# Kernel optimization log

Hardware: AMD Instinct MI355X
Metric: run time of the kernel (lower is better)

Reference implementation:

```python
import jax, jax.numpy as jnp
import numpy as np

N = 20000   # nodes
E = 320000  # edges
G = 64      # graphs in batch
IN = 256    # in_dim
H = 256     # hidden_dim1
C = 2       # n_classes


def setup_inputs() -> dict:
    key = jax.random.key(0)
    ks = jax.random.split(key, 12)
    h = jax.random.normal(ks[0], (N, IN), jnp.float32)
    src = jax.random.randint(ks[1], (E,), 0, N)
    dst = jax.random.randint(ks[2], (E,), 0, N)
    graph_id = jnp.sort(jax.random.randint(ks[3], (N,), 0, G))
    s_in = 1.0 / np.sqrt(IN)
    s_h = 1.0 / np.sqrt(H)
    W_conv = jax.random.normal(ks[4], (IN, H), jnp.float32) * s_in
    b_conv = jnp.zeros((H,), jnp.float32)
    w_gate = jax.random.normal(ks[5], (H, 1), jnp.float32) * s_h
    b_gate = jnp.zeros((1,), jnp.float32)
    W1 = jax.random.normal(ks[6], (H, H), jnp.float32) * s_h
    b1 = jnp.zeros((H,), jnp.float32)
    W2 = jax.random.normal(ks[7], (H, C), jnp.float32) * s_h
    b2 = jnp.zeros((C,), jnp.float32)
    return dict(h=h, src=src, dst=dst, graph_id=graph_id, W_conv=W_conv,
                b_conv=b_conv, w_gate=w_gate, b_gate=b_gate, W1=W1, b1=b1,
                W2=W2, b2=b2)


def reference(h, src, dst, graph_id, W_conv, b_conv, w_gate, b_gate, W1, b1, W2, b2):
    ones_e = jnp.ones((E,), jnp.float32)
    # DGL GraphConv, norm='both': D_out^-1/2 on source, D_in^-1/2 on dest
    deg_out = jax.ops.segment_sum(ones_e, src, num_segments=N)
    deg_in = jax.ops.segment_sum(ones_e, dst, num_segments=N)
    hn = h * jax.lax.rsqrt(jnp.maximum(deg_out, 1.0))[:, None]
    hn = hn @ W_conv                       # [N, H] (weight applied before aggregation)
    agg = jax.ops.segment_sum(hn[src], dst, num_segments=N)  # gather + scatter-add
    agg = agg * jax.lax.rsqrt(jnp.maximum(deg_in, 1.0))[:, None] + b_conv
    hr = jax.nn.relu(agg)                  # F.relu after conv1
    # GlobalAttentionPooling: per-graph segment softmax over gate scores
    gate = hr @ w_gate + b_gate            # [N, 1]
    gmax = jax.ops.segment_max(gate, graph_id, num_segments=G)
    e = jnp.exp(gate - gmax[graph_id])
    denom = jax.ops.segment_sum(e, graph_id, num_segments=G)
    att = e / denom[graph_id]              # [N, 1] attention weights (g2)
    hg = jax.ops.segment_sum(att * hr, graph_id, num_segments=G)  # [G, H]
    # classifier heads (dropout is identity at inference)
    a2 = hg @ W1 + b1
    a3 = a2 @ W2 + b2
    return jax.nn.sigmoid(a3), att, hg
```

## Files before the change

kernel.cpp:

```cpp
#include <hip/hip_runtime.h>
#include <hip/hip_bf16.h>
#include <hip/hip_fp16.h>
#include <math.h>

#define NN 20000
#define EE 320000
#define GG 64
#define IND 256
#define HD 256
#define CC 2

#define HRB 32
#define EPB (EE/HRB)
#define NH  (NN/2)

typedef __hip_bfloat16 bf16;
typedef __attribute__((ext_vector_type(8))) short short8;
typedef __attribute__((ext_vector_type(4))) float f32x4;

__device__ __forceinline__ float b2f(bf16 x){ return __bfloat162float(x); }
__device__ __forceinline__ float bits2f(unsigned short b){
    union{ float f; unsigned u; } v; v.u = ((unsigned)b) << 16; return v.f;
}
__device__ __forceinline__ short f2bs(float x){
    union{ bf16 b; short s; } u; u.b = __float2bfloat16(x); return u.s;
}
__device__ __forceinline__ float ldf3(const void* p, size_t i, int c){
    if (c == 1) return b2f(((const bf16*)p)[i]);
    if (c == 2) return __half2float(((const __half*)p)[i]);
    return ((const float*)p)[i];
}
__device__ __forceinline__ int idec(const void* p, int i, int c){
    if (c == 1) return (int)(((const long long*)p)[i]);
    if (c == 2) return (int)(((const float*)p)[i]);
    if (c == 3) return (int)__half2float(((const __half*)p)[i]);
    return ((const int*)p)[i];
}
__device__ __forceinline__ int wdetect_wave(const unsigned short* p, int t){
    unsigned u = p[2*t];
    int e8 = (u >> 7) & 0xFF;
    int e5 = (u >> 10) & 0x1F;
    int nz = __popcll(__ballot(u != 0));
    int cb = __popcll(__ballot(e8 >= 100 && e8 <= 141));
    int cf = __popcll(__ballot(e5 >= 4 && e5 <= 22));
    return (nz < 8) ? 0 : (cb >= 60) ? 1 : ((cf >= 60) ? 2 : 0);
}

#define ZBLK 8
#define DETB (9 + IND)
__global__ __launch_bounds__(256) void k_detect(const void* src, const void* dst,
                         const void* gid,
                         const unsigned short* h, const unsigned short* Wc,
                         const unsigned short* wg, const unsigned short* W1,
                         const unsigned short* W2, const unsigned short* bc,
                         int* icode, int* dcode, int* zero_base,
                         bf16* __restrict__ Wb){
    int blk = blockIdx.x;
    int t = threadIdx.x;
    if (blk < 3){
        if (t >= 64) return;
        const void* buf = (blk == 0) ? src : (blk == 1) ? dst : gid;
        int n     = (blk == 2) ? NN : EE;
        int bound = (blk == 2) ? GG : NN;
        long long v64 = ((const long long*)buf)[n/8 + t];
        unsigned long long bad64 = __ballot(v64 < 0 || v64 >= (long long)bound);
        int v32 = ((const int*)buf)[n/4 + t];
        unsigned long long bad32 = __ballot(v32 < 0 || v32 >= bound);
        float f32v = __uint_as_float(((const unsigned*)buf)[n/4 + t]);
        unsigned long long badf32 = __ballot(!(f32v >= 0.f && f32v < (float)bound));
        float f16v = __half2float(((const __half*)buf)[n/2 + t]);
        unsigned long long badf16 = __ballot(!(f16v >= 0.f && f16v < (float)bound));
        if (t == 0)
            icode[blk] = (bad64 == 0ull) ? 1 : ((bad32 == 0ull) ? 0 :
                         ((badf32 == 0ull) ? 2 : ((badf16 == 0ull) ? 3 : 0)));
    } else if (blk < 9){
        if (t >= 64) return;
        int b = blk - 3;
        const unsigned short* p = b==0?h:b==1?Wc:b==2?wg:b==3?W1:b==4?W2:bc;
        int code = wdetect_wave(p, t);
        if (t == 0) dcode[b] = code;
    } else if (blk < DETB){
        int k = blk - 9;
        __shared__ int scode;
        if (t < 64){
            int code = wdetect_wave(Wc, t);
            if (t == 0) scode = code;
        }
        __syncthreads();
        int c = scode;
        Wb[(size_t)t*IND + k] = __float2bfloat16(ldf3(Wc, (size_t)k*HD + t, c));
    } else {
        int idx = (blk - DETB)*256 + t;
        const int total = GG*HD;
        for (int i = idx; i < total; i += ZBLK*256) zero_base[i] = 0;
    }
}

#define GEMMB (NN/32)
__global__ __launch_bounds__(256) void k_prepgemm(const void* __restrict__ h,
                                                  const bf16* __restrict__ Wb,
                                                  const void* __restrict__ src_r,
                                                  const void* __restrict__ dst_r,
                                                  const int* __restrict__ icode,
                                                  const int* __restrict__ dcode,
                                                  int* __restrict__ pout,
                                                  int* __restrict__ pin,
                                                  bf16* __restrict__ hn){
    __shared__ int shm[NH];
    int blk = blockIdx.x;
    int tid = threadIdx.x;
    if (blk >= GEMMB){
        int hb = blk - GEMMB;
        int hr = hb >> 2, role = (hb >> 1) & 1, half = hb & 1;
        for (int i = tid; i < NH; i += 256) shm[i] = 0;
        __syncthreads();
        const void* arr = role ? dst_r : src_r;
        int code = icode[role];
        int base = hr*EPB;
        for (int e = base + tid; e < base + EPB; e += 256){
            int v = idec(arr, e, code);
            int vh = v - half*NH;
            if ((unsigned)vh < NH) atomicAdd(&shm[vh], 1);
        }
        __syncthreads();
        int* dst_part = (role ? pin : pout) + (size_t)hr*NN + half*NH;
        for (int i = tid; i < NH; i += 256) dst_part[i] = shm[i];
        return;
    }
    unsigned short* tile = (unsigned short*)shm;
    int fh = dcode[0];
    int wave = tid >> 6, lane = tid & 63;
    int q = lane >> 4, mr = lane & 15;
    int row0 = blk * 32;
    int ncol0 = wave * 64;
    f32x4 acc[2][4] = {};
    const float* hf = (const float*)h;
    #pragma unroll
    for (int k0 = 0; k0 < IND; k0 += 32){
        short8 a[2], b[4];
        if (fh == 0){
            #pragma unroll
            for (int mi = 0; mi < 2; mi++){
                int r = row0 + mi*16 + mr;
                const float4* p = (const float4*)(hf + (size_t)r*IND + k0 + q*8);
                float4 v0 = p[0], v1 = p[1];
                a[mi][0] = f2bs(v0.x); a[mi][1] = f2bs(v0.y);
                a[mi][2] = f2bs(v0.z); a[mi][3] = f2bs(v0.w);
                a[mi][4] = f2bs(v1.x); a[mi][5] = f2bs(v1.y);
                a[mi][6] = f2bs(v1.z); a[mi][7] = f2bs(v1.w);
            }
        } else {
            #pragma unroll
            for (int mi = 0; mi < 2; mi++){
                int r = row0 + mi*16 + mr;
                #pragma unroll
                for (int j = 0; j < 8; j++)
                    a[mi][j] = f2bs(ldf3(h, (size_t)r*IND + k0 + q*8 + j, fh));
            }
        }
        #pragma unroll
        for (int ni = 0; ni < 4; ni++)
            b[ni] = *reinterpret_cast<const short8*>(
                        Wb + (size_t)(ncol0 + ni*16 + mr)*IND + k0 + q*8);
        #pragma unroll
        for (int mi = 0; mi < 2; mi++)
            #pragma unroll
            for (int ni = 0; ni < 4; ni++)
                acc[mi][ni] = __builtin_amdgcn_mfma_f32_16x16x32_bf16(
                                  a[mi], b[ni], acc[mi][ni], 0, 0, 0);
    }
    #pragma unroll
    for (int mi = 0; mi < 2; mi++){
        int rowb = mi*16 + q*4;
        #pragma unroll
        for (int r = 0; r < 4; r++){
            int row = rowb + r;
            #pragma unroll
            for (int ni = 0; ni < 4; ni++)
                tile[row*260 + ncol0 + ni*16 + mr] =
                    (unsigned short)f2bs(acc[mi][ni][r]);
        }
    }
    __syncthreads();
    #pragma unroll
    for (int p = 0; p < 4; p++){
        int s = p*256 + tid;
        int row = s >> 5;
        int c8 = (s & 31) * 8;
        short8 v = *reinterpret_cast<const short8*>(&tile[row*260 + c8]);
        *reinterpret_cast<short8*>(hn + (size_t)(row0 + row)*HD + c8) = v;
    }
}

__global__ __launch_bounds__(256) void k_red(const void* __restrict__ gid_r,
                                             const int* __restrict__ icode,
                                             int* __restrict__ pout,
                                             int* __restrict__ pin,
                                             float* __restrict__ rs_o,
                                             float* __restrict__ rs_i,
                                             int* __restrict__ cnt_in,
                                             int* __restrict__ gid_i){
    int n = blockIdx.x*256 + threadIdx.x;
    if (n >= NN) return;
    int so = 0;
    #pragma unroll 8
    for (int hr = 0; hr < HRB; hr++) so += pout[(size_t)hr*NN + n];
    rs_o[n] = rsqrtf(fmaxf((float)so, 1.f));
    int pre = 0;
    #pragma unroll 8
    for (int hr = 0; hr < HRB; hr++){
        int v = pin[(size_t)hr*NN + n];
        pin[(size_t)hr*NN + n] = pre;
        pre += v;
    }
    cnt_in[n] = pre;
    rs_i[n] = rsqrtf(fmaxf((float)pre, 1.f));
    gid_i[n] = idec(gid_r, n, icode[2]);
}

__global__ __launch_bounds__(1024) void k_scan(const int* __restrict__ cnt_in,
                                               const int* __restrict__ gid,
                                               int* __restrict__ row_start,
                                               int* gstart, int* gend){
    int t = threadIdx.x;
    __shared__ int part[1024];
    const int per = (NN + 1023)/1024;
    int lo = t*per, hi = min(lo+per, NN);
    int s = 0;
    for (int i = lo; i < hi; i++) s += cnt_in[i];
    part[t] = s; __syncthreads();
    for (int off = 1; off < 1024; off <<= 1){
        int v = (t >= off) ? part[t-off] : 0;
        __syncthreads();
        part[t] += v;
        __syncthreads();
    }
    int base = part[t] - s;
    for (int i = lo; i < hi; i++){ row_start[i] = base; base += cnt_in[i]; }
    if (t == 1023) row_start[NN] = part[1023];
    __shared__ int ls[GG+1];
    if (t <= GG){
        int a = 0, b = NN;
        while (a < b){
            int mid = (a + b) >> 1;
            if (gid[mid] < t) a = mid + 1; else b = mid;
        }
        ls[t] = a;
    }
    __syncthreads();
    if (t < GG){ gstart[t] = ls[t]; gend[t] = ls[t+1]; }
}

__global__ __launch_bounds__(256) void k_fill(const void* src_r, const void* dst_r,
                       const int* __restrict__ icode,
                       const int* __restrict__ row_start,
                       const int* __restrict__ pin,
                       int* __restrict__ csr_src){
    __shared__ int lr[NH];
    int blk = blockIdx.x, t = threadIdx.x;
    int hr = blk >> 1, half = blk & 1;
    for (int i = t; i < NH; i += 256) lr[i] = 0;
    __syncthreads();
    int c0 = icode[0], c1 = icode[1];
    int base = hr*EPB;
    const int* pre = pin + (size_t)hr*NN;
    for (int e = base + t; e < base + EPB; e += 256){
        int s = idec(src_r, e, c0);
        int d = idec(dst_r, e, c1);
        if ((unsigned)s >= NN || (unsigned)d >= NN) continue;
        int dh = d - half*NH;
        if ((unsigned)dh < NH){
            int r = atomicAdd(&lr[dh], 1);
            csr_src[row_start[d] + pre[d] + r] = s;
        }
    }
}

__global__ __launch_bounds__(256) void k_gather(const bf16* __restrict__ hn,
                                                const float* __restrict__ rs_out,
                                                const float* __restrict__ rs_in,
                                                const int* __restrict__ row_start,
                                                const int* __restrict__ csr_src,
                                                const void* __restrict__ b_conv,
                                                const void* __restrict__ w_gate,
                                                const void* __restrict__ b_gate,
                                                const int* __restrict__ dcode,
                                                float* __restrict__ hr,
                                                float* __restrict__ gate){
    int wave = threadIdx.x >> 6, lane = threadIdx.x & 63;
    int n = blockIdx.x*4 + wave;
    if (n >= NN) return;
    int lo = row_start[n], hi = row_start[n+1];
    int half = lane >> 5, l2 = lane & 31;
    float a0=0.f,a1=0.f,a2=0.f,a3=0.f,a4=0.f,a5=0.f,a6=0.f,a7=0.f;
    int j = lo;
    for (; j + 8 <= hi; j += 8){
        int sA = csr_src[j+0+half], sB = csr_src[j+2+half];
        int sC = csr_src[j+4+half], sD = csr_src[j+6+half];
        float rA = rs_out[sA], rB = rs_out[sB], rC = rs_out[sC], rD = rs_out[sD];
        short8 uA = *reinterpret_cast<const short8*>(hn + (size_t)sA*HD + l2*8);
        short8 uB = *reinterpret_cast<const short8*>(hn + (size_t)sB*HD + l2*8);
        short8 uC = *reinterpret_cast<const short8*>(hn + (size_t)sC*HD + l2*8);
        short8 uD = *reinterpret_cast<const short8*>(hn + (size_t)sD*HD + l2*8);
        a0 = fmaf(rA, bits2f((unsigned short)uA[0]),
             fmaf(rB, bits2f((unsigned short)uB[0]),
             fmaf(rC, bits2f((unsigned short)uC[0]),
             fmaf(rD, bits2f((unsigned short)uD[0]), a0))));
        a1 = fmaf(rA, bits2f((unsigned short)uA[1]),
             fmaf(rB, bits2f((unsigned short)uB[1]),
             fmaf(rC, bits2f((unsigned short)uC[1]),
             fmaf(rD, bits2f((unsigned short)uD[1]), a1))));
        a2 = fmaf(rA, bits2f((unsigned short)uA[2]),
             fmaf(rB, bits2f((unsigned short)uB[2]),
             fmaf(rC, bits2f((unsigned short)uC[2]),
             fmaf(rD, bits2f((unsigned short)uD[2]), a2))));
        a3 = fmaf(rA, bits2f((unsigned short)uA[3]),
             fmaf(rB, bits2f((unsigned short)uB[3]),
             fmaf(rC, bits2f((unsigned short)uC[3]),
             fmaf(rD, bits2f((unsigned short)uD[3]), a3))));
        a4 = fmaf(rA, bits2f((unsigned short)uA[4]),
             fmaf(rB, bits2f((unsigned short)uB[4]),
             fmaf(rC, bits2f((unsigned short)uC[4]),
             fmaf(rD, bits2f((unsigned short)uD[4]), a4))));
        a5 = fmaf(rA, bits2f((unsigned short)uA[5]),
             fmaf(rB, bits2f((unsigned short)uB[5]),
             fmaf(rC, bits2f((unsigned short)uC[5]),
             fmaf(rD, bits2f((unsigned short)uD[5]), a5))));
        a6 = fmaf(rA, bits2f((unsigned short)uA[6]),
             fmaf(rB, bits2f((unsigned short)uB[6]),
             fmaf(rC, bits2f((unsigned short)uC[6]),
             fmaf(rD, bits2f((unsigned short)uD[6]), a6))));
        a7 = fmaf(rA, bits2f((unsigned short)uA[7]),
             fmaf(rB, bits2f((unsigned short)uB[7]),
             fmaf(rC, bits2f((unsigned short)uC[7]),
             fmaf(rD, bits2f((unsigned short)uD[7]), a7))));
    }
    for (; j + 2 <= hi; j += 2){
        int s = csr_src[j+half];
        float r = rs_out[s];
        short8 u = *reinterpret_cast<const short8*>(hn + (size_t)s*HD + l2*8);
        a0 = fmaf(r, bits2f((unsigned short)u[0]), a0);
        a1 = fmaf(r, bits2f((unsigned short)u[1]), a1);
        a2 = fmaf(r, bits2f((unsigned short)u[2]), a2);
        a3 = fmaf(r, bits2f((unsigned short)u[3]), a3);
        a4 = fmaf(r, bits2f((unsigned short)u[4]), a4);
        a5 = fmaf(r, bits2f((unsigned short)u[5]), a5);
        a6 = fmaf(r, bits2f((unsigned short)u[6]), a6);
        a7 = fmaf(r, bits2f((unsigned short)u[7]), a7);
    }
    if (j < hi && half == 0){
        int s = csr_src[j];
        float r = rs_out[s];
        short8 u = *reinterpret_cast<const short8*>(hn + (size_t)s*HD + l2*8);
        a0 = fmaf(r, bits2f((unsigned short)u[0]), a0);
        a1 = fmaf(r, bits2f((unsigned short)u[1]), a1);
        a2 = fmaf(r, bits2f((unsigned short)u[2]), a2);
        a3 = fmaf(r, bits2f((unsigned short)u[3]), a3);
        a4 = fmaf(r, bits2f((unsigned short)u[4]), a4);
        a5 = fmaf(r, bits2f((unsigned short)u[5]), a5);
        a6 = fmaf(r, bits2f((unsigned short)u[6]), a6);
        a7 = fmaf(r, bits2f((unsigned short)u[7]), a7);
    }
    float send0 = half ? a0 : a4;
    float send1 = half ? a1 : a5;
    float send2 = half ? a2 : a6;
    float send3 = half ? a3 : a7;
    float recv0 = __shfl_xor(send0, 32);
    float recv1 = __shfl_xor(send1, 32);
    float recv2 = __shfl_xor(send2, 32);
    float recv3 = __shfl_xor(send3, 32);
    float tot0 = (half ? a4 : a0) + recv0;
    float tot1 = (half ? a5 : a1) + recv1;
    float tot2 = (half ? a6 : a2) + recv2;
    float tot3 = (half ? a7 : a3) + recv3;
    int db = dcode[5], fg = dcode[2];
    float rsn = rs_in[n];
    int c = l2*8 + half*4;
    float v0 = fmaxf(fmaf(tot0, rsn, ldf3(b_conv, c+0, db)), 0.f);
    float v1 = fmaxf(fmaf(tot1, rsn, ldf3(b_conv, c+1, db)), 0.f);
    float v2 = fmaxf(fmaf(tot2, rsn, ldf3(b_conv, c+2, db)), 0.f);
    float v3 = fmaxf(fmaf(tot3, rsn, ldf3(b_conv, c+3, db)), 0.f);
    float4 fv; fv.x = v0; fv.y = v1; fv.z = v2; fv.w = v3;
    *(float4*)(hr + (size_t)n*HD + c) = fv;
    float g = v0*ldf3(w_gate, c+0, fg) + v1*ldf3(w_gate, c+1, fg)
            + v2*ldf3(w_gate, c+2, fg) + v3*ldf3(w_gate, c+3, fg);
    #pragma unroll
    for (int off = 32; off; off >>= 1) g += __shfl_down(g, off);
    if (lane == 0) gate[n] = g + ldf3(b_gate, 0, db);
}

__global__ __launch_bounds__(256) void k_softhg(const float* __restrict__ gate,
                                                const float* __restrict__ hr,
                                                const int* __restrict__ gstart,
                                                const int* __restrict__ gend,
                                                float* __restrict__ hg,
                                                float* __restrict__ out_att){
    int g = blockIdx.x >> 3, part = blockIdx.x & 7;
    int t = threadIdx.x, lane = t & 63, wid = t >> 6;
    int lo = gstart[g], hi = gend[g], len = hi - lo;
    if (len <= 0) return;
    __shared__ float red[4];
    float m = -INFINITY;
    for (int n = lo + t; n < hi; n += 256) m = fmaxf(m, gate[n]);
    #pragma unroll
    for (int off = 32; off; off >>= 1) m = fmaxf(m, __shfl_xor(m, off));
    if (lane == 0) red[wid] = m;
    __syncthreads();
    m = fmaxf(fmaxf(red[0], red[1]), fmaxf(red[2], red[3]));
    __syncthreads();
    float s = 0.f;
    for (int n = lo + t; n < hi; n += 256) s += expf(gate[n] - m);
    #pragma unroll
    for (int off = 32; off; off >>= 1) s += __shfl_xor(s, off);
    if (lane == 0) red[wid] = s;
    __syncthreads();
    s = red[0] + red[1] + red[2] + red[3];
    float inv = 1.f / s;
    int chunk = (len + 7) >> 3;
    int plo = lo + part*chunk, phi = min(plo + chunk, hi);
    if (plo >= phi) return;
    for (int n = plo + t; n < phi; n += 256)
        out_att[n] = expf(gate[n] - m) * inv;
    float a0 = 0.f, a1 = 0.f, a2 = 0.f, a3 = 0.f;
    int r = plo;
    for (; r + 4 <= phi; r += 4){
        float w0 = expf(gate[r+0] - m) * inv;
        float w1 = expf(gate[r+1] - m) * inv;
        float w2 = expf(gate[r+2] - m) * inv;
        float w3 = expf(gate[r+3] - m) * inv;
        a0 = fmaf(w0, hr[(size_t)(r+0)*HD + t], a0);
        a1 = fmaf(w1, hr[(size_t)(r+1)*HD + t], a1);
        a2 = fmaf(w2, hr[(size_t)(r+2)*HD + t], a2);
        a3 = fmaf(w3, hr[(size_t)(r+3)*HD + t], a3);
    }
    for (; r < phi; r++)
        a0 = fmaf(expf(gate[r] - m) * inv, hr[(size_t)r*HD + t], a0);
    atomicAdd(&hg[g*HD + t], (a0 + a1) + (a2 + a3));
}

__global__ __launch_bounds__(256) void k_cls(const float* __restrict__ hg,
                                             const void* __restrict__ W1,
                                             const void* __restrict__ b1,
                                             const void* __restrict__ W2,
                                             const void* __restrict__ b2,
                                             const int* __restrict__ dcode,
                                             float* __restrict__ out0,
                                             float* __restrict__ out_hg){
    int f1 = dcode[3], f2 = dcode[4], db = dcode[5];
    int g = blockIdx.x, tid = threadIdx.x;
    __shared__ float hs[256];
    float hv = hg[g*HD + tid];
    hs[tid] = hv;
    out_hg[g*HD + tid] = hv;
    __syncthreads();
    float acc = ldf3(b1, tid, db);
    if (f1 == 1){
        const bf16* w = (const bf16*)W1;
        for (int k = 0; k < HD; k++) acc += hs[k]*b2f(w[(size_t)k*HD + tid]);
    } else if (f1 == 2){
        const __half* w = (const __half*)W1;
        for (int k = 0; k < HD; k++) acc += hs[k]*__half2float(w[(size_t)k*HD + tid]);
    } else {
        const float* w = (const float*)W1;
        for (int k = 0; k < HD; k++) acc += hs[k]*w[(size_t)k*HD + tid];
    }
    float p0 = acc * ldf3(W2, tid*CC + 0, f2);
    float p1 = acc * ldf3(W2, tid*CC + 1, f2);
    __shared__ float r0[256], r1[256];
    r0[tid] = p0; r1[tid] = p1; __syncthreads();
    for (int s = 128; s; s >>= 1){
        if (tid < s){ r0[tid] += r0[tid+s]; r1[tid] += r1[tid+s]; }
        __syncthreads();
    }
    if (tid == 0){
        out0[g*CC+0] = 1.f/(1.f + expf(-(r0[0] + ldf3(b2, 0, db))));
        out0[g*CC+1] = 1.f/(1.f + expf(-(r1[0] + ldf3(b2, 1, db))));
    }
}

extern "C" void kernel_launch(void* const* d_in, const int* in_sizes, int n_in,
                              void* d_out, int out_size, void* d_ws, size_t ws_size,
                              hipStream_t stream) {
    const void* h      = d_in[0];
    const void* src_r  = d_in[1];
    const void* dst_r  = d_in[2];
    const void* gid_r  = d_in[3];
    const void* W_conv = d_in[4];
    const void* b_conv = d_in[5];
    const void* w_gate = d_in[6];
    const void* b_gate = d_in[7];
    const void* W1     = d_in[8];
    const void* b1     = d_in[9];
    const void* W2     = d_in[10];
    const void* b2     = d_in[11];

    float* out     = (float*)d_out;
    float* out0    = out;
    float* out_att = out + GG*CC;
    float* out_hg  = out + GG*CC + NN;

    char* w = (char*)d_ws;
    float* hr   = (float*)w;  w += (size_t)NN*HD*sizeof(float);
    bf16*  hn   = (bf16*)w;   w += (size_t)NN*HD*sizeof(bf16);
    bf16*  Wb   = (bf16*)w;   w += (size_t)IND*HD*sizeof(bf16);
    float* rs_o = (float*)w;  w += (size_t)NN*sizeof(float);
    float* rs_i = (float*)w;  w += (size_t)NN*sizeof(float);
    float* gate = (float*)w;  w += (size_t)NN*sizeof(float);
    int* gstart = (int*)w;    w += GG*sizeof(int);
    int* gend   = (int*)w;    w += GG*sizeof(int);
    int* dcode  = (int*)w;    w += 8*sizeof(int);
    int* icode  = (int*)w;    w += 8*sizeof(int);
    int* gid_i  = (int*)w;    w += (size_t)NN*sizeof(int);
    int* cnt_in = (int*)w;    w += (size_t)NN*sizeof(int);
    float* hg   = (float*)w;  w += (size_t)GG*HD*sizeof(float);
    int* rowst  = (int*)w;    w += (size_t)(NN+1)*sizeof(int);
    int* csr    = (int*)w;    w += (size_t)EE*sizeof(int);
    int* pout   = (int*)w;    w += (size_t)HRB*NN*sizeof(int);
    int* pin    = (int*)w;    w += (size_t)HRB*NN*sizeof(int);

    k_detect<<<DETB + ZBLK, 256, 0, stream>>>(src_r, dst_r, gid_r,
                                     (const unsigned short*)h, (const unsigned short*)W_conv,
                                     (const unsigned short*)w_gate, (const unsigned short*)W1,
                                     (const unsigned short*)W2, (const unsigned short*)b_conv,
                                     icode, dcode, hg ? (int*)hg : nullptr, Wb);

    k_prepgemm<<<GEMMB + HRB*4, 256, 0, stream>>>(h, Wb, src_r, dst_r,
                                                  icode, dcode, pout, pin, hn);

    k_red<<<(NN+255)/256, 256, 0, stream>>>(gid_r, icode, pout, pin,
                                            rs_o, rs_i, cnt_in, gid_i);

    k_scan<<<1, 1024, 0, stream>>>(cnt_in, gid_i, rowst, gstart, gend);

    k_fill<<<HRB*2, 256, 0, stream>>>(src_r, dst_r, icode, rowst, pin, csr);

    k_gather<<<(NN+3)/4, 256, 0, stream>>>(hn, rs_o, rs_i, rowst, csr,
                                           b_conv, w_gate, b_gate, dcode, hr, gate);

    k_softhg<<<GG*8, 256, 0, stream>>>(gate, hr, gstart, gend, hg, out_att);

    k_cls<<<GG, 256, 0, stream>>>(hg, W1, b1, W2, b2, dcode, out0, out_hg);
}
```

Before: 223.2 us.

## Move degree histograms into detect kernel and fuse degree reduction with GEMM

The per-chunk degree histogram blocks move from the GEMM kernel into the detect kernel, and each block detects the index dtype itself. The degree reduction kernel is merged into the GEMM launch as extra blocks, which removes one kernel launch and its serialization point. The detect kernel now declares 40KB of shared memory for every block, which may lower its occupancy.

```diff
diff --git a/kernel.cpp b/kernel.cpp
--- a/kernel.cpp
+++ b/kernel.cpp
@@ -45,6 +45,18 @@
     int cf = __popcll(__ballot(e5 >= 4 && e5 <= 22));
     return (nz < 8) ? 0 : (cb >= 60) ? 1 : ((cf >= 60) ? 2 : 0);
 }
+__device__ __forceinline__ int idetect_wave(const void* buf, int n, int bound, int t){
+    long long v64 = ((const long long*)buf)[n/8 + t];
+    unsigned long long bad64 = __ballot(v64 < 0 || v64 >= (long long)bound);
+    int v32 = ((const int*)buf)[n/4 + t];
+    unsigned long long bad32 = __ballot(v32 < 0 || v32 >= bound);
+    float f32v = __uint_as_float(((const unsigned*)buf)[n/4 + t]);
+    unsigned long long badf32 = __ballot(!(f32v >= 0.f && f32v < (float)bound));
+    float f16v = __half2float(((const __half*)buf)[n/2 + t]);
+    unsigned long long badf16 = __ballot(!(f16v >= 0.f && f16v < (float)bound));
+    return (bad64 == 0ull) ? 1 : ((bad32 == 0ull) ? 0 :
+           ((badf32 == 0ull) ? 2 : ((badf16 == 0ull) ? 3 : 0)));
+}
 
 #define ZBLK 8
 #define DETB (9 + IND)
@@ -54,7 +66,10 @@
                          const unsigned short* wg, const unsigned short* W1,
                          const unsigned short* W2, const unsigned short* bc,
                          int* icode, int* dcode, int* zero_base,
-                         bf16* __restrict__ Wb){
+                         bf16* __restrict__ Wb,
+                         int* __restrict__ pout, int* __restrict__ pin){
+    __shared__ int shm[NH];
+    __shared__ int scode;
     int blk = blockIdx.x;
     int t = threadIdx.x;
     if (blk < 3){
@@ -62,17 +77,8 @@
         const void* buf = (blk == 0) ? src : (blk == 1) ? dst : gid;
         int n     = (blk == 2) ? NN : EE;
         int bound = (blk == 2) ? GG : NN;
-        long long v64 = ((const long long*)buf)[n/8 + t];
-        unsigned long long bad64 = __ballot(v64 < 0 || v64 >= (long long)bound);
-        int v32 = ((const int*)buf)[n/4 + t];
-        unsigned long long bad32 = __ballot(v32 < 0 || v32 >= bound);
-        float f32v = __uint_as_float(((const unsigned*)buf)[n/4 + t]);
-        unsigned long long badf32 = __ballot(!(f32v >= 0.f && f32v < (float)bound));
-        float f16v = __half2float(((const __half*)buf)[n/2 + t]);
-        unsigned long long badf16 = __ballot(!(f16v >= 0.f && f16v < (float)bound));
-        if (t == 0)
-            icode[blk] = (bad64 == 0ull) ? 1 : ((bad32 == 0ull) ? 0 :
-                         ((badf32 == 0ull) ? 2 : ((badf16 == 0ull) ? 3 : 0)));
+        int code = idetect_wave(buf, n, bound, t);
+        if (t == 0) icode[blk] = code;
     } else if (blk < 9){
         if (t >= 64) return;
         int b = blk - 3;
@@ -81,7 +87,6 @@
         if (t == 0) dcode[b] = code;
     } else if (blk < DETB){
         int k = blk - 9;
-        __shared__ int scode;
         if (t < 64){
             int code = wdetect_wave(Wc, t);
             if (t == 0) scode = code;
@@ -89,45 +94,69 @@
         __syncthreads();
         int c = scode;
         Wb[(size_t)t*IND + k] = __float2bfloat16(ldf3(Wc, (size_t)k*HD + t, c));
+    } else if (blk < DETB + HRB*4){
+        int hb = blk - DETB;
+        int hr = hb >> 2, role = (hb >> 1) & 1, half = hb & 1;
+        const void* arr = role ? dst : src;
+        if (t < 64){
+            int code = idetect_wave(arr, EE, NN, t);
+            if (t == 0) scode = code;
+        }
+        for (int i = t; i < NH; i += 256) shm[i] = 0;
+        __syncthreads();
+        int code = scode;
+        int base = hr*EPB;
+        for (int e = base + t; e < base + EPB; e += 256){
+            int v = idec(arr, e, code);
+            int vh = v - half*NH;
+            if ((unsigned)vh < NH) atomicAdd(&shm[vh], 1);
+        }
+        __syncthreads();
+        int* dst_part = (role ? pin : pout) + (size_t)hr*NN + half*NH;
+        for (int i = t; i < NH; i += 256) dst_part[i] = shm[i];
     } else {
-        int idx = (blk - DETB)*256 + t;
+        int idx = (blk - (DETB + HRB*4))*256 + t;
         const int total = GG*HD;
         for (int i = idx; i < total; i += ZBLK*256) zero_base[i] = 0;
     }
 }
 
 #define GEMMB (NN/32)
-__global__ __launch_bounds__(256) void k_prepgemm(const void* __restrict__ h,
-                                                  const bf16* __restrict__ Wb,
-                                                  const void* __restrict__ src_r,
-                                                  const void* __restrict__ dst_r,
-                                                  const int* __restrict__ icode,
-                                                  const int* __restrict__ dcode,
-                                                  int* __restrict__ pout,
-                                                  int* __restrict__ pin,
-                                                  bf16* __restrict__ hn){
-    __shared__ int shm[NH];
+#define REDB ((NN+255)/256)
+__global__ __launch_bounds__(256) void k_gemmred(const void* __restrict__ h,
+                                                 const bf16* __restrict__ Wb,
+                                                 const void* __restrict__ gid_r,
+                                                 const int* __restrict__ icode,
+                                                 const int* __restrict__ dcode,
+                                                 int* __restrict__ pout,
+                                                 int* __restrict__ pin,
+                                                 float* __restrict__ rs_o,
+                                                 float* __restrict__ rs_i,
+                                                 int* __restrict__ cnt_in,
+                                                 int* __restrict__ gid_i,
+                                                 bf16* __restrict__ hn){
+    __shared__ unsigned short tile[32*260];
     int blk = blockIdx.x;
     int tid = threadIdx.x;
     if (blk >= GEMMB){
-        int hb = blk - GEMMB;
-        int hr = hb >> 2, role = (hb >> 1) & 1, half = hb & 1;
-        for (int i = tid; i < NH; i += 256) shm[i] = 0;
-        __syncthreads();
-        const void* arr = role ? dst_r : src_r;
-        int code = icode[role];
-        int base = hr*EPB;
-        for (int e = base + tid; e < base + EPB; e += 256){
-            int v = idec(arr, e, code);
-            int vh = v - half*NH;
-            if ((unsigned)vh < NH) atomicAdd(&shm[vh], 1);
-        }
-        __syncthreads();
-        int* dst_part = (role ? pin : pout) + (size_t)hr*NN + half*NH;
-        for (int i = tid; i < NH; i += 256) dst_part[i] = shm[i];
+        int n = (blk - GEMMB)*256 + tid;
+        if (n >= NN) return;
+        int so = 0;
+        #pragma unroll 8
+        for (int hr = 0; hr < HRB; hr++) so += pout[(size_t)hr*NN + n];
+        rs_o[n] = rsqrtf(fmaxf((float)so, 1.f));
+        int pre = 0;
+        #pragma unroll 8
+        for (int hr = 0; hr < HRB; hr++){
+            int v = pin[(size_t)hr*NN + n];
+            pin[(size_t)hr*NN + n] = pre;
+            pre += v;
+        }
+        cnt_in[n] = pre;
+        rs_i[n] = rsqrtf(fmaxf((float)pre, 1.f));
+        gid_i[n] = idec(gid_r, n, icode[2]);
         return;
     }
-    unsigned short* tile = (unsigned short*)shm;
     int fh = dcode[0];
     int wave = tid >> 6, lane = tid & 63;
     int q = lane >> 4, mr = lane & 15;
@@ -190,32 +219,6 @@
         short8 v = *reinterpret_cast<const short8*>(&tile[row*260 + c8]);
         *reinterpret_cast<short8*>(hn + (size_t)(row0 + row)*HD + c8) = v;
     }
-}
-
-__global__ __launch_bounds__(256) void k_red(const void* __restrict__ gid_r,
-                                             const int* __restrict__ icode,
-                                             int* __restrict__ pout,
-                                             int* __restrict__ pin,
-                                             float* __restrict__ rs_o,
-                                             float* __restrict__ rs_i,
-                                             int* __restrict__ cnt_in,
-                                             int* __restrict__ gid_i){
-    int n = blockIdx.x*256 + threadIdx.x;
-    if (n >= NN) return;
-    int so = 0;
-    #pragma unroll 8
-    for (int hr = 0; hr < HRB; hr++) so += pout[(size_t)hr*NN + n];
-    rs_o[n] = rsqrtf(fmaxf((float)so, 1.f));
-    int pre = 0;
-    #pragma unroll 8
-    for (int hr = 0; hr < HRB; hr++){
-        int v = pin[(size_t)hr*NN + n];
-        pin[(size_t)hr*NN + n] = pre;
-        pre += v;
-    }
-    cnt_in[n] = pre;
-    rs_i[n] = rsqrtf(fmaxf((float)pre, 1.f));
-    gid_i[n] = idec(gid_r, n, icode[2]);
 }
 
 __global__ __launch_bounds__(1024) void k_scan(const int* __restrict__ cnt_in,
@@ -518,17 +521,15 @@
     int* pout   = (int*)w;    w += (size_t)HRB*NN*sizeof(int);
     int* pin    = (int*)w;    w += (size_t)HRB*NN*sizeof(int);
 
-    k_detect<<<DETB + ZBLK, 256, 0, stream>>>(src_r, dst_r, gid_r,
+    k_detect<<<DETB + HRB*4 + ZBLK, 256, 0, stream>>>(src_r, dst_r, gid_r,
                                      (const unsigned short*)h, (const unsigned short*)W_conv,
                                      (const unsigned short*)w_gate, (const unsigned short*)W1,
                                      (const unsigned short*)W2, (const unsigned short*)b_conv,
-                                     icode, dcode, hg ? (int*)hg : nullptr, Wb);
-
-    k_prepgemm<<<GEMMB + HRB*4, 256, 0, stream>>>(h, Wb, src_r, dst_r,
-                                                  icode, dcode, pout, pin, hn);
-
-    k_red<<<(NN+255)/256, 256, 0, stream>>>(gid_r, icode, pout, pin,
-                                            rs_o, rs_i, cnt_in, gid_i);
+                                     icode, dcode, (int*)hg, Wb, pout, pin);
+
+    k_gemmred<<<GEMMB + REDB, 256, 0, stream>>>(h, Wb, gid_r, icode, dcode,
+                                                pout, pin, rs_o, rs_i,
+                                                cnt_in, gid_i, hn);
 
     k_scan<<<1, 1024, 0, stream>>>(cnt_in, gid_i, rowst, gstart, gend);
 
```

Measured after the change: 232.1 us. 1.04x slower.
